# Performance work log

Hardware: AMD Instinct MI355X
Metric: run time of the kernel (lower is better)

The kernel has to match this reference:

```python
import jax, jax.numpy as jnp
import numpy as np

B, CIN, H, W = 16, 15, 256, 256
C, L, M = 64, 4, 16
ENV, D1D = 40, 4
HEAD_IN = C + ENV + D1D
BN_EPS = 1e-5


def setup_inputs() -> dict:
    key = jax.random.key(0)
    ks = iter(jax.random.split(key, 40))
    nrm = lambda shape: jax.random.normal(next(ks), shape, dtype=jnp.float32)
    scale = (2.0 / (C + C)) ** 0.5
    uni = lambda shape: scale * (jax.random.uniform(next(ks), shape, dtype=jnp.float32) - 0.5)
    d = {
        'grid': nrm((B, CIN, H, W)),
        'env': nrm((B, ENV)),
        'd1d': nrm((B, D1D)),
        'lift_w': nrm((C, CIN)) * 0.1, 'lift_b': nrm((C,)) * 0.01,
        'w1r': uni((L, C, C, M, M)), 'w1i': uni((L, C, C, M, M)),
        'w2r': uni((L, C, C, M, M)), 'w2i': uni((L, C, C, M, M)),
        'skip_w': nrm((L, C, C)) * 0.1, 'skip_b': nrm((L, C)) * 0.01,
        'bn_g': jnp.ones((L, C)), 'bn_b': jnp.zeros((L, C)),
        'bn_m': nrm((L, C)) * 0.01, 'bn_v': jnp.abs(nrm((L, C))) * 0.1 + 1.0,
        'proj_w': nrm((C, C)) * 0.1, 'proj_b': nrm((C,)) * 0.01,
        'dw1': nrm((128, HEAD_IN)) * 0.05, 'db1': nrm((128,)) * 0.01,
        'dw2': nrm((64, 128)) * 0.05, 'db2': nrm((64,)) * 0.01,
        'dw3': nrm((8, 64)) * 0.05, 'db3': nrm((8,)) * 0.01,
        'iw1': nrm((128, HEAD_IN)) * 0.05, 'ib1': nrm((128,)) * 0.01,
        'iw2': nrm((64, 128)) * 0.05, 'ib2': nrm((64,)) * 0.01,
        'iw3': nrm((4, 64)) * 0.05, 'ib3': nrm((4,)) * 0.01,
    }
    return d


def _spectral(x, w1, w2):
    # x: [B,C,H,W] real; w1,w2: [C,C,M,M] complex
    h, w = x.shape[-2], x.shape[-1]
    xft = jnp.fft.rfft2(x)  # [B,C,H,W//2+1] complex
    top = jnp.einsum('bixy,ioxy->boxy', xft[:, :, :M, :M], w1)
    bot = jnp.einsum('bixy,ioxy->boxy', xft[:, :, -M:, :M], w2)
    out_ft = jnp.zeros(xft.shape, dtype=xft.dtype)
    out_ft = out_ft.at[:, :, :M, :M].set(top).at[:, :, h - M:, :M].set(bot)
    return jnp.fft.irfft2(out_ft, s=(h, w))


def _conv1x1(x, w, b):
    return jnp.einsum('bchw,oc->bohw', x, w) + b[None, :, None, None]


def _gelu(x):
    return jax.nn.gelu(x, approximate=False)


def reference(grid, env, d1d, lift_w, lift_b, w1r, w1i, w2r, w2i, skip_w, skip_b,
              bn_g, bn_b, bn_m, bn_v, proj_w, proj_b,
              dw1, db1, dw2, db2, dw3, db3, iw1, ib1, iw2, ib2, iw3, ib3):
    x = _gelu(_conv1x1(grid, lift_w, lift_b))
    for l in range(L):
        residual = x
        w1 = w1r[l] + 1j * w1i[l]
        w2 = w2r[l] + 1j * w2i[l]
        y = _spectral(x, w1, w2) + _conv1x1(x, skip_w[l], skip_b[l])
        # BatchNorm2d in eval mode (running stats), dropout is identity at eval
        y = (y - bn_m[l][None, :, None, None]) * jax.lax.rsqrt(bn_v[l] + BN_EPS)[None, :, None, None]
        y = y * bn_g[l][None, :, None, None] + bn_b[l][None, :, None, None]
        x = _gelu(y) + residual
    x = _gelu(_conv1x1(x, proj_w, proj_b))
    x = x.mean(axis=(-2, -1))  # [B,C]
    x = jnp.concatenate([x, env, d1d], axis=-1)  # [B, C+44]
    h = _gelu(x @ dw1.T + db1)
    h = _gelu(h @ dw2.T + db2)
    out_dir = h @ dw3.T + db3
    g = _gelu(x @ iw1.T + ib1)
    g = _gelu(g @ iw2.T + ib2)
    out_int = g @ iw3.T + ib3
    return out_dir, out_int
```

## Files before the change

### kernel.cpp

```cpp
#include <hip/hip_runtime.h>
#include <hip/hip_bf16.h>
#include <math.h>

#define B_ 16
#define CIN_ 15
#define C_ 64
#define L_ 4

typedef __attribute__((ext_vector_type(8))) short short8;
typedef __attribute__((ext_vector_type(4))) float f32x4;

__device__ __forceinline__ float gelu_f(float x) {
    float z = fabsf(x) * 0.70710678118654752440f;
    float t = __builtin_amdgcn_rcpf(fmaf(0.3275911f, z, 1.0f));
    float p = t * fmaf(t, fmaf(t, fmaf(t, fmaf(t, 1.061405429f, -1.453152027f), 1.421413741f), -0.284496736f), 0.254829592f);
    float e = __expf(-z * z);
    float E = fmaf(-p, e, 1.0f);
    return 0.5f * fmaf(fabsf(x), E, x);
}

__device__ __forceinline__ unsigned short f2bf(float x) {
    __hip_bfloat16 h = __float2bfloat16(x);
    return *(unsigned short*)&h;
}
__device__ __forceinline__ float bf2f(unsigned short u) {
    __hip_bfloat16 h = *(__hip_bfloat16*)&u;
    return __bfloat162float(h);
}
__device__ __forceinline__ f32x4 mfma16(short8 a, short8 b, f32x4 c) {
    return __builtin_amdgcn_mfma_f32_16x16x32_bf16(a, b, c, 0, 0, 0);
}

#define TWO_PI_OVER_256 0.024543692606170259674f

__global__ __launch_bounds__(256) void k_prep(const float* __restrict__ skip_w,
                                              const float* __restrict__ bn_g, const float* __restrict__ bn_v,
                                              const float* __restrict__ proj_w,
                                              unsigned short* __restrict__ TfH, unsigned short* __restrict__ TfL,
                                              unsigned short* __restrict__ TiH, unsigned short* __restrict__ TiL,
                                              unsigned short* __restrict__ WH, unsigned short* __restrict__ WL,
                                              unsigned short* __restrict__ PH, unsigned short* __restrict__ PL) {
    int id = blockIdx.x * 256 + threadIdx.x;
    if (id < 8192) {
        int col = id >> 8, w = id & 255;
        int kk = (col < 16) ? col : (col - 16);
        float s, c;
        sincosf(TWO_PI_OVER_256 * (float)((w * kk) & 255), &s, &c);
        float v = (col < 16) ? c : -s;
        unsigned short hi = f2bf(v);
        TfH[id] = hi; TfL[id] = f2bf(v - bf2f(hi));
    } else if (id < 16384) {
        int idx = id - 8192;
        int w = idx >> 5, k = idx & 31, ky = k >> 1;
        float s, c;
        sincosf(TWO_PI_OVER_256 * (float)((w * ky) & 255), &s, &c);
        float v = (k & 1) ? -s : c;
        unsigned short hi = f2bf(v);
        TiH[idx] = hi; TiL[idx] = f2bf(v - bf2f(hi));
    } else if (id < 32768) {
        int idx = id - 16384;
        int lco = idx >> 6;
        float scl = bn_g[lco] * rsqrtf(bn_v[lco] + 1e-5f);
        float v = scl * skip_w[idx];
        unsigned short hi = f2bf(v);
        WH[idx] = hi; WL[idx] = f2bf(v - bf2f(hi));
    } else if (id < 36864) {
        int idx = id - 32768;
        float v = proj_w[idx];
        unsigned short hi = f2bf(v);
        PH[idx] = hi; PL[idx] = f2bf(v - bf2f(hi));
    }
}

__global__ __launch_bounds__(256) void k_lift(const float* __restrict__ g, const float* __restrict__ lw,
                                              const float* __restrict__ lb, unsigned short* __restrict__ X,
                                              const unsigned short* __restrict__ TfH, const unsigned short* __restrict__ TfL,
                                              float2* __restrict__ Y) {
    __shared__ float gs[CIN_][256];
    __shared__ float lws[C_ * CIN_];
    __shared__ float lbs[C_];
    __shared__ unsigned short xl[64 * 264];
    int b = blockIdx.x >> 8, h = blockIdx.x & 255;
    int t = threadIdx.x;
    for (int ci = 0; ci < CIN_; ci++)
        gs[ci][t] = g[((b * CIN_ + ci) * 256 + h) * 256 + t];
    for (int idx = t; idx < C_ * CIN_; idx += 256) lws[idx] = lw[idx];
    if (t < C_) lbs[t] = lb[t];
    __syncthreads();
    for (int co = 0; co < C_; co++) {
        float acc = lbs[co];
        #pragma unroll
        for (int ci = 0; ci < CIN_; ci++) acc += gs[ci][t] * lws[co * CIN_ + ci];
        xl[co * 264 + t] = f2bf(gelu_f(acc));
    }
    __syncthreads();
    {
        int wv = t >> 6, ln = t & 63;
        int lx = ln & 15, q = ln >> 4;
        f32x4 fa0 = {0.f, 0.f, 0.f, 0.f}, fa1 = {0.f, 0.f, 0.f, 0.f};
        for (int ks = 0; ks < 8; ks++) {
            int k0 = ks * 32;
            short8 a = *(const short8*)(&xl[(wv * 16 + lx) * 264 + k0 + q * 8]);
            short8 bh0 = *(const short8*)(TfH + lx * 256 + k0 + q * 8);
            short8 bl0 = *(const short8*)(TfL + lx * 256 + k0 + q * 8);
            short8 bh1 = *(const short8*)(TfH + (16 + lx) * 256 + k0 + q * 8);
            short8 bl1 = *(const short8*)(TfL + (16 + lx) * 256 + k0 + q * 8);
            fa0 = mfma16(a, bh0, fa0); fa0 = mfma16(a, bl0, fa0);
            fa1 = mfma16(a, bh1, fa1); fa1 = mfma16(a, bl1, fa1);
        }
        #pragma unroll
        for (int r = 0; r < 4; r++) {
            int c = wv * 16 + q * 4 + r;
            Y[(b * 64 + c) * 4096 + h * 16 + lx] = make_float2(fa0[r], fa1[r]);
        }
    }
    unsigned short* Xg = X + (size_t)(b * 64) * 65536 + h * 256;
    #pragma unroll
    for (int r = 0; r < 8; r++) {
        int idx = r * 256 + t;
        int c = idx >> 5, w8 = idx & 31;
        *(short8*)(Xg + c * 65536 + w8 * 8) = *(const short8*)(&xl[c * 264 + w8 * 8]);
    }
}

__global__ __launch_bounds__(256) void k_fwd_h(const float2* __restrict__ Y, float2* __restrict__ XF) {
    __shared__ float2 yl[4096];
    __shared__ float tc[256], ts[256];
    int bc = blockIdx.x;
    int t = threadIdx.x;
    {
        float s, c;
        sincosf((float)t * TWO_PI_OVER_256, &s, &c);
        tc[t] = c; ts[t] = s;
    }
    for (int idx = t; idx < 4096; idx += 256) yl[idx] = Y[bc * 4096 + idx];
    __syncthreads();
    int j = t & 31, kg = t >> 5;
    int kxu = j + ((j < 16) ? 0 : 224);
    int b = bc >> 6, c = bc & 63;
    for (int q = 0; q < 2; q++) {
        int ky = kg * 2 + q;
        float xre = 0.f, xim = 0.f;
        int m = 0;
        #pragma unroll 8
        for (int h = 0; h < 256; h++) {
            float2 yv = yl[h * 16 + ky];
            float cc = tc[m], ss = ts[m];
            xre += yv.x * cc + yv.y * ss;
            xim += yv.y * cc - yv.x * ss;
            m = (m + kxu) & 255;
        }
        XF[(j * 16 + ky) * 1024 + b * 64 + c] = make_float2(xre, xim);
    }
}

__global__ __launch_bounds__(256) void k_repack(const float* __restrict__ w1r, const float* __restrict__ w1i,
                                                const float* __restrict__ w2r, const float* __restrict__ w2i,
                                                float2* __restrict__ WPK, int l) {
    int id = blockIdx.x * 256 + threadIdx.x;
    int ky = id & 15;
    int o  = (id >> 4) & 63;
    int i  = (id >> 10) & 63;
    int j  = id >> 16;
    int x  = j & 15;
    const float* wr = (j < 16) ? w1r : w2r;
    const float* wi = (j < 16) ? w1i : w2i;
    int src = ((l * 64 + i) * 64 + o) * 256 + x * 16 + ky;
    int dst = ((j * 16 + ky) * 64 + i) * 64 + o;
    WPK[dst] = make_float2(wr[src], wi[src]);
}

__global__ __launch_bounds__(256) void k_mix(const float2* __restrict__ XF, const float2* __restrict__ WPK,
                                             float2* __restrict__ YF) {
    __shared__ float2 xs[1024];
    __shared__ float2 wls[4096];
    int s = blockIdx.x;
    int t = threadIdx.x;
    for (int idx = t; idx < 1024; idx += 256) xs[idx] = XF[s * 1024 + idx];
    for (int idx = t; idx < 4096; idx += 256) wls[idx] = WPK[(size_t)s * 4096 + idx];
    __syncthreads();
    int o = t & 63, bg = t >> 6;
    float2 acc[4];
    #pragma unroll
    for (int q = 0; q < 4; q++) acc[q] = make_float2(0.f, 0.f);
    for (int i = 0; i < 64; i++) {
        float2 wv = wls[i * 64 + o];
        #pragma unroll
        for (int q = 0; q < 4; q++) {
            float2 xv = xs[(bg * 4 + q) * 64 + i];
            acc[q].x += xv.x * wv.x - xv.y * wv.y;
            acc[q].y += xv.x * wv.y + xv.y * wv.x;
        }
    }
    #pragma unroll
    for (int q = 0; q < 4; q++) {
        int b = bg * 4 + q;
        YF[(b * 64 + o) * 512 + s] = acc[q];
    }
}

__global__ __launch_bounds__(256) void k_inv_h(const float2* __restrict__ YF, float2* __restrict__ Z) {
    __shared__ float2 yl[512];
    __shared__ float tc[256], ts[256];
    int bc = blockIdx.x, t = threadIdx.x;
    {
        float s, c;
        sincosf((float)t * TWO_PI_OVER_256, &s, &c);
        tc[t] = c; ts[t] = s;
    }
    for (int idx = t; idx < 512; idx += 256) yl[idx] = YF[bc * 512 + idx];
    __syncthreads();
    float zr[16], zi[16];
    #pragma unroll
    for (int ky = 0; ky < 16; ky++) { zr[ky] = 0.f; zi[ky] = 0.f; }
    for (int j = 0; j < 32; j++) {
        int kxu = j + ((j < 16) ? 0 : 224);
        int m = (t * kxu) & 255;
        float cc = tc[m], ss = ts[m];
        #pragma unroll
        for (int ky = 0; ky < 16; ky++) {
            float2 yv = yl[j * 16 + ky];
            zr[ky] += yv.x * cc - yv.y * ss;
            zi[ky] += yv.x * ss + yv.y * cc;
        }
    }
    int base = bc * 4096 + t * 16;
    #pragma unroll
    for (int ky = 0; ky < 16; ky++) Z[base + ky] = make_float2(zr[ky], zi[ky]);
}

__global__ __launch_bounds__(256) void k_tail(unsigned short* __restrict__ X, const float2* __restrict__ Z,
                                              const unsigned short* __restrict__ WH, const unsigned short* __restrict__ WL,
                                              const float* __restrict__ sbl, const float* __restrict__ bng,
                                              const float* __restrict__ bnb, const float* __restrict__ bnm,
                                              const float* __restrict__ bnv,
                                              const unsigned short* __restrict__ TiH, const unsigned short* __restrict__ TiL,
                                              const unsigned short* __restrict__ TfH, const unsigned short* __restrict__ TfL,
                                              float2* __restrict__ Y, int mode,
                                              const unsigned short* __restrict__ PH, const unsigned short* __restrict__ PL,
                                              const float* __restrict__ pb, float* __restrict__ ACC) {
    __shared__ unsigned short xl[64 * 264];
    __shared__ float cbs[64];
    __shared__ float pacc[64];
    __shared__ float pbs[64];
    int b = blockIdx.x >> 8, h = blockIdx.x & 255;
    int t = threadIdx.x;
    unsigned short* Xg = X + (size_t)(b * 64) * 65536 + h * 256;
    #pragma unroll
    for (int r = 0; r < 8; r++) {
        int idx = r * 256 + t;
        int c = idx >> 5, w8 = idx & 31;
        *(short8*)(&xl[c * 264 + w8 * 8]) = *(const short8*)(Xg + c * 65536 + w8 * 8);
    }
    if (t < 64) {
        float scl = bng[t] * rsqrtf(bnv[t] + 1e-5f);
        cbs[t] = scl * (sbl[t] - bnm[t]) + bnb[t];
        pacc[t] = 0.f;
        pbs[t] = pb[t];
    }
    __syncthreads();

    int wv = t >> 6, ln = t & 63;
    int lx = ln & 15, q = ln >> 4;

    short8 azh[4], azl[4];
    {
        const float2* Zg = Z + (size_t)(b * 64) * 4096 + h * 16;
        #pragma unroll
        for (int mt = 0; mt < 4; mt++) {
            int co = mt * 16 + lx;
            float scl = bng[co] * rsqrtf(bnv[co] + 1e-5f);
            float f2v = scl * (2.0f / 65536.0f);
            float f0 = (q == 0) ? (scl * (1.0f / 65536.0f)) : f2v;
            const float4* zp = (const float4*)(Zg + (size_t)co * 4096 + q * 4);
            float4 z0 = zp[0], z1 = zp[1];
            float v[8];
            v[0] = z0.x * f0;  v[1] = z0.y * f0;
            v[2] = z0.z * f2v; v[3] = z0.w * f2v;
            v[4] = z1.x * f2v; v[5] = z1.y * f2v;
            v[6] = z1.z * f2v; v[7] = z1.w * f2v;
            #pragma unroll
            for (int j = 0; j < 8; j++) {
                unsigned short hv = f2bf(v[j]);
                azh[mt][j] = (short)hv;
                azl[mt][j] = (short)f2bf(v[j] - bf2f(hv));
            }
        }
    }

    #pragma unroll 1
    for (int nt = 0; nt < 4; nt++) {
        int w = wv * 64 + nt * 16 + lx;
        f32x4 acc[4];
        #pragma unroll
        for (int mt = 0; mt < 4; mt++) acc[mt] = (f32x4){0.f, 0.f, 0.f, 0.f};
        {
            short8 tbh = *(const short8*)(TiH + w * 32 + q * 8);
            short8 tbl = *(const short8*)(TiL + w * 32 + q * 8);
            #pragma unroll
            for (int mt = 0; mt < 4; mt++) {
                acc[mt] = mfma16(azh[mt], tbh, acc[mt]);
                acc[mt] = mfma16(azh[mt], tbl, acc[mt]);
                acc[mt] = mfma16(azl[mt], tbh, acc[mt]);
            }
        }
        #pragma unroll
        for (int ks = 0; ks < 2; ks++) {
            int k0 = ks * 32;
            short8 bfr;
            #pragma unroll
            for (int j = 0; j < 8; j++)
                bfr[j] = (short)xl[(k0 + q * 8 + j) * 264 + w];
            #pragma unroll
            for (int mt = 0; mt < 4; mt++) {
                short8 ah = *(const short8*)(WH + (mt * 16 + lx) * 64 + k0 + q * 8);
                short8 al = *(const short8*)(WL + (mt * 16 + lx) * 64 + k0 + q * 8);
                acc[mt] = mfma16(ah, bfr, acc[mt]);
                acc[mt] = mfma16(al, bfr, acc[mt]);
            }
        }
        #pragma unroll
        for (int mt = 0; mt < 4; mt++) {
            #pragma unroll
            for (int r = 0; r < 4; r++) {
                int co = mt * 16 + q * 4 + r;
                float y = acc[mt][r] + cbs[co];
                float v = gelu_f(y) + bf2f(xl[co * 264 + w]);
                xl[co * 264 + w] = f2bf(v);
            }
        }
    }
    __syncthreads();

    if (mode == 1) {
        f32x4 fa0 = {0.f, 0.f, 0.f, 0.f}, fa1 = {0.f, 0.f, 0.f, 0.f};
        for (int ks = 0; ks < 8; ks++) {
            int k0 = ks * 32;
            short8 a = *(const short8*)(&xl[(wv * 16 + lx) * 264 + k0 + q * 8]);
            short8 bh0 = *(const short8*)(TfH + lx * 256 + k0 + q * 8);
            short8 bl0 = *(const short8*)(TfL + lx * 256 + k0 + q * 8);
            short8 bh1 = *(const short8*)(TfH + (16 + lx) * 256 + k0 + q * 8);
            short8 bl1 = *(const short8*)(TfL + (16 + lx) * 256 + k0 + q * 8);
            fa0 = mfma16(a, bh0, fa0); fa0 = mfma16(a, bl0, fa0);
            fa1 = mfma16(a, bh1, fa1); fa1 = mfma16(a, bl1, fa1);
        }
        #pragma unroll
        for (int r = 0; r < 4; r++) {
            int c = wv * 16 + q * 4 + r;
            Y[(b * 64 + c) * 4096 + h * 16 + lx] = make_float2(fa0[r], fa1[r]);
        }
        #pragma unroll
        for (int r = 0; r < 8; r++) {
            int idx = r * 256 + t;
            int c = idx >> 5, w8 = idx & 31;
            *(short8*)(Xg + c * 65536 + w8 * 8) = *(const short8*)(&xl[c * 264 + w8 * 8]);
        }
    } else {
        float psum[4][4];
        #pragma unroll
        for (int mt = 0; mt < 4; mt++)
            #pragma unroll
            for (int r = 0; r < 4; r++) psum[mt][r] = 0.f;
        #pragma unroll 1
        for (int nt = 0; nt < 4; nt++) {
            int w = wv * 64 + nt * 16 + lx;
            f32x4 acc[4];
            #pragma unroll
            for (int mt = 0; mt < 4; mt++) acc[mt] = (f32x4){0.f, 0.f, 0.f, 0.f};
            #pragma unroll
            for (int ks = 0; ks < 2; ks++) {
                int k0 = ks * 32;
                short8 bfr;
                #pragma unroll
                for (int j = 0; j < 8; j++)
                    bfr[j] = (short)xl[(k0 + q * 8 + j) * 264 + w];
                #pragma unroll
                for (int mt = 0; mt < 4; mt++) {
                    short8 ah = *(const short8*)(PH + (mt * 16 + lx) * 64 + k0 + q * 8);
                    short8 al = *(const short8*)(PL + (mt * 16 + lx) * 64 + k0 + q * 8);
                    acc[mt] = mfma16(ah, bfr, acc[mt]);
                    acc[mt] = mfma16(al, bfr, acc[mt]);
                }
            }
            #pragma unroll
            for (int mt = 0; mt < 4; mt++)
                #pragma unroll
                for (int r = 0; r < 4; r++) {
                    int co = mt * 16 + q * 4 + r;
                    psum[mt][r] += gelu_f(acc[mt][r] + pbs[co]);
                }
        }
        #pragma unroll
        for (int mt = 0; mt < 4; mt++) {
            #pragma unroll
            for (int r = 0; r < 4; r++) {
                int co = mt * 16 + q * 4 + r;
                float s = psum[mt][r];
                s += __shfl_xor(s, 1, 64);
                s += __shfl_xor(s, 2, 64);
                s += __shfl_xor(s, 4, 64);
                s += __shfl_xor(s, 8, 64);
                if (lx == 0) atomicAdd(&pacc[co], s);
            }
        }
        __syncthreads();
        if (t < 64) atomicAdd(&ACC[b * 64 + t], pacc[t]);
    }
}

__global__ __launch_bounds__(128) void k_head(const float* __restrict__ ACC, const float* __restrict__ env,
                                              const float* __restrict__ d1d,
                                              const float* __restrict__ dw1, const float* __restrict__ db1,
                                              const float* __restrict__ dw2, const float* __restrict__ db2,
                                              const float* __restrict__ dw3, const float* __restrict__ db3,
                                              const float* __restrict__ iw1, const float* __restrict__ ib1,
                                              const float* __restrict__ iw2, const float* __restrict__ ib2,
                                              const float* __restrict__ iw3, const float* __restrict__ ib3,
                                              float* __restrict__ out) {
    __shared__ float xc[108];
    __shared__ float h1[128];
    __shared__ float h2[64];
    int b = blockIdx.x, t = threadIdx.x;
    if (t < 64) xc[t] = ACC[b * 64 + t] * (1.0f / 65536.0f);
    else if (t < 104) xc[t] = env[b * 40 + (t - 64)];
    else if (t < 108) xc[t] = d1d[b * 4 + (t - 104)];
    __syncthreads();
    {
        float a = db1[t];
        for (int k = 0; k < 108; k++) a += xc[k] * dw1[t * 108 + k];
        h1[t] = gelu_f(a);
    }
    __syncthreads();
    if (t < 64) {
        float a = db2[t];
        for (int k = 0; k < 128; k++) a += h1[k] * dw2[t * 128 + k];
        h2[t] = gelu_f(a);
    }
    __syncthreads();
    if (t < 8) {
        float a = db3[t];
        for (int k = 0; k < 64; k++) a += h2[k] * dw3[t * 64 + k];
        out[b * 8 + t] = a;
    }
    __syncthreads();
    {
        float a = ib1[t];
        for (int k = 0; k < 108; k++) a += xc[k] * iw1[t * 108 + k];
        h1[t] = gelu_f(a);
    }
    __syncthreads();
    if (t < 64) {
        float a = ib2[t];
        for (int k = 0; k < 128; k++) a += h1[k] * iw2[t * 128 + k];
        h2[t] = gelu_f(a);
    }
    __syncthreads();
    if (t < 4) {
        float a = ib3[t];
        for (int k = 0; k < 64; k++) a += h2[k] * iw3[t * 64 + k];
        out[128 + b * 4 + t] = a;
    }
}

extern "C" void kernel_launch(void* const* d_in, const int* in_sizes, int n_in,
                              void* d_out, int out_size, void* d_ws, size_t ws_size,
                              hipStream_t stream) {
    const float* grid_  = (const float*)d_in[0];
    const float* env    = (const float*)d_in[1];
    const float* d1d    = (const float*)d_in[2];
    const float* lift_w = (const float*)d_in[3];
    const float* lift_b = (const float*)d_in[4];
    const float* w1r    = (const float*)d_in[5];
    const float* w1i    = (const float*)d_in[6];
    const float* w2r    = (const float*)d_in[7];
    const float* w2i    = (const float*)d_in[8];
    const float* skip_w = (const float*)d_in[9];
    const float* skip_b = (const float*)d_in[10];
    const float* bn_g   = (const float*)d_in[11];
    const float* bn_b   = (const float*)d_in[12];
    const float* bn_m   = (const float*)d_in[13];
    const float* bn_v   = (const float*)d_in[14];
    const float* proj_w = (const float*)d_in[15];
    const float* proj_b = (const float*)d_in[16];
    const float* dw1 = (const float*)d_in[17];
    const float* db1 = (const float*)d_in[18];
    const float* dw2 = (const float*)d_in[19];
    const float* db2 = (const float*)d_in[20];
    const float* dw3 = (const float*)d_in[21];
    const float* db3 = (const float*)d_in[22];
    const float* iw1 = (const float*)d_in[23];
    const float* ib1 = (const float*)d_in[24];
    const float* iw2 = (const float*)d_in[25];
    const float* ib2 = (const float*)d_in[26];
    const float* iw3 = (const float*)d_in[27];
    const float* ib3 = (const float*)d_in[28];

    char* ws = (char*)d_ws;
    unsigned short* X   = (unsigned short*)(ws);
    float2* S   = (float2*)(ws + 134217728);
    float2* XF  = (float2*)(ws + 167772160);
    float2* YF  = (float2*)(ws + 171966464);
    float2* WPK = (float2*)(ws + 176160768);
    float*  ACC = (float*)(ws + 192937984);
    unsigned short* TfH = (unsigned short*)(ws + 192942080);
    unsigned short* TfL = (unsigned short*)(ws + 192958464);
    unsigned short* TiH = (unsigned short*)(ws + 192974848);
    unsigned short* TiL = (unsigned short*)(ws + 192991232);
    unsigned short* WH  = (unsigned short*)(ws + 193007616);
    unsigned short* WL  = (unsigned short*)(ws + 193040384);
    unsigned short* PH  = (unsigned short*)(ws + 193073152);
    unsigned short* PL  = (unsigned short*)(ws + 193081344);

    hipMemsetAsync(ACC, 0, 1024 * sizeof(float), stream);
    k_prep<<<144, 256, 0, stream>>>(skip_w, bn_g, bn_v, proj_w, TfH, TfL, TiH, TiL, WH, WL, PH, PL);
    k_lift<<<4096, 256, 0, stream>>>(grid_, lift_w, lift_b, X, TfH, TfL, S);
    for (int l = 0; l < L_; l++) {
        k_repack<<<8192, 256, 0, stream>>>(w1r, w1i, w2r, w2i, WPK, l);
        k_fwd_h<<<1024, 256, 0, stream>>>(S, XF);
        k_mix<<<512, 256, 0, stream>>>(XF, WPK, YF);
        k_inv_h<<<1024, 256, 0, stream>>>(YF, S);
        k_tail<<<4096, 256, 0, stream>>>(X, S, WH + l * 4096, WL + l * 4096,
                                         skip_b + l * 64, bn_g + l * 64, bn_b + l * 64,
                                         bn_m + l * 64, bn_v + l * 64,
                                         TiH, TiL, TfH, TfL, S, (l < 3) ? 1 : 2,
                                         PH, PL, proj_b, ACC);
    }
    k_head<<<16, 128, 0, stream>>>(ACC, env, d1d, dw1, db1, dw2, db2, dw3, db3,
                                   iw1, ib1, iw2, ib2, iw3, ib3, (float*)d_out);
}
```

Baseline: 1.380 ms.

## Move H-axis partial DFTs onto bf16 MFMA with split-precision twiddle tables

The forward and inverse H-direction DFT kernels are rewritten from scalar FMA loops over LDS twiddles to bf16x3 split-precision MFMA matrix products. The cos, sin and negated-sin twiddle matrices are precomputed in hi/lo bf16 form by the prep kernel. The forward kernel splits the 256-long H reduction across four waves and sums their partials in shared memory. The weight repack kernel is also changed to process four outputs per thread with vectorized float4 stores. The goal is to cut FP32 ALU time in the DFT stages, at the cost of extra precomputed tables and bf16 split rounding error.

```diff
diff --git a/kernel.cpp b/kernel.cpp
--- a/kernel.cpp
+++ b/kernel.cpp
@@ -39,7 +39,13 @@
                                               unsigned short* __restrict__ TfH, unsigned short* __restrict__ TfL,
                                               unsigned short* __restrict__ TiH, unsigned short* __restrict__ TiL,
                                               unsigned short* __restrict__ WH, unsigned short* __restrict__ WL,
-                                              unsigned short* __restrict__ PH, unsigned short* __restrict__ PL) {
+                                              unsigned short* __restrict__ PH, unsigned short* __restrict__ PL,
+                                              unsigned short* __restrict__ FcH, unsigned short* __restrict__ FcL,
+                                              unsigned short* __restrict__ FsH, unsigned short* __restrict__ FsL,
+                                              unsigned short* __restrict__ FnH, unsigned short* __restrict__ FnL,
+                                              unsigned short* __restrict__ IcH, unsigned short* __restrict__ IcL,
+                                              unsigned short* __restrict__ IsH, unsigned short* __restrict__ IsL,
+                                              unsigned short* __restrict__ InH, unsigned short* __restrict__ InL) {
     int id = blockIdx.x * 256 + threadIdx.x;
     if (id < 8192) {
         int col = id >> 8, w = id & 255;
@@ -69,6 +75,30 @@
         float v = proj_w[idx];
         unsigned short hi = f2bf(v);
         PH[idx] = hi; PL[idx] = f2bf(v - bf2f(hi));
+    } else if (id < 45056) {
+        int idx = id - 36864;
+        int j = idx >> 8, h = idx & 255;
+        int kxu = j + ((j < 16) ? 0 : 224);
+        float s, c;
+        sincosf(TWO_PI_OVER_256 * (float)((h * kxu) & 255), &s, &c);
+        unsigned short ch = f2bf(c);
+        FcH[idx] = ch; FcL[idx] = f2bf(c - bf2f(ch));
+        unsigned short sh = f2bf(s);
+        unsigned short sl = f2bf(s - bf2f(sh));
+        FsH[idx] = sh; FsL[idx] = sl;
+        FnH[idx] = sh ^ 0x8000; FnL[idx] = sl ^ 0x8000;
+    } else if (id < 53248) {
+        int idx = id - 45056;
+        int h = idx >> 5, j = idx & 31;
+        int kxu = j + ((j < 16) ? 0 : 224);
+        float s, c;
+        sincosf(TWO_PI_OVER_256 * (float)((h * kxu) & 255), &s, &c);
+        unsigned short ch = f2bf(c);
+        IcH[idx] = ch; IcL[idx] = f2bf(c - bf2f(ch));
+        unsigned short sh = f2bf(s);
+        unsigned short sl = f2bf(s - bf2f(sh));
+        IsH[idx] = sh; IsL[idx] = sl;
+        InH[idx] = sh ^ 0x8000; InL[idx] = sl ^ 0x8000;
     }
 }
 
@@ -123,51 +153,93 @@
     }
 }
 
-__global__ __launch_bounds__(256) void k_fwd_h(const float2* __restrict__ Y, float2* __restrict__ XF) {
-    __shared__ float2 yl[4096];
-    __shared__ float tc[256], ts[256];
+__global__ __launch_bounds__(256) void k_fwd_h(const float2* __restrict__ Y, float2* __restrict__ XF,
+                                               const unsigned short* __restrict__ FcH, const unsigned short* __restrict__ FcL,
+                                               const unsigned short* __restrict__ FsH, const unsigned short* __restrict__ FsL,
+                                               const unsigned short* __restrict__ FnH, const unsigned short* __restrict__ FnL) {
+    __shared__ float red[4][2][2][64][4];
     int bc = blockIdx.x;
     int t = threadIdx.x;
-    {
-        float s, c;
-        sincosf((float)t * TWO_PI_OVER_256, &s, &c);
-        tc[t] = c; ts[t] = s;
-    }
-    for (int idx = t; idx < 4096; idx += 256) yl[idx] = Y[bc * 4096 + idx];
-    __syncthreads();
-    int j = t & 31, kg = t >> 5;
-    int kxu = j + ((j < 16) ? 0 : 224);
-    int b = bc >> 6, c = bc & 63;
-    for (int q = 0; q < 2; q++) {
-        int ky = kg * 2 + q;
-        float xre = 0.f, xim = 0.f;
-        int m = 0;
-        #pragma unroll 8
-        for (int h = 0; h < 256; h++) {
-            float2 yv = yl[h * 16 + ky];
-            float cc = tc[m], ss = ts[m];
-            xre += yv.x * cc + yv.y * ss;
-            xim += yv.y * cc - yv.x * ss;
-            m = (m + kxu) & 255;
-        }
-        XF[(j * 16 + ky) * 1024 + b * 64 + c] = make_float2(xre, xim);
+    int wv = t >> 6, l = t & 63, lx = l & 15, g = l >> 4;
+    const float2* Yb = Y + (size_t)bc * 4096;
+    f32x4 aR[2], aI[2];
+    aR[0] = (f32x4){0.f,0.f,0.f,0.f}; aR[1] = aR[0]; aI[0] = aR[0]; aI[1] = aR[0];
+    #pragma unroll
+    for (int kk = 0; kk < 2; kk++) {
+        int ks = wv * 2 + kk;
+        short8 yrh, yrl, yih, yil;
+        #pragma unroll
+        for (int j = 0; j < 8; j++) {
+            float2 v = Yb[(ks * 32 + g * 8 + j) * 16 + lx];
+            unsigned short h1 = f2bf(v.x);
+            yrh[j] = (short)h1; yrl[j] = (short)f2bf(v.x - bf2f(h1));
+            unsigned short h2 = f2bf(v.y);
+            yih[j] = (short)h2; yil[j] = (short)f2bf(v.y - bf2f(h2));
+        }
+        #pragma unroll
+        for (int rt = 0; rt < 2; rt++) {
+            int base = (rt * 16 + lx) * 256 + ks * 32 + g * 8;
+            short8 ch = *(const short8*)(FcH + base);
+            short8 cl = *(const short8*)(FcL + base);
+            short8 sh = *(const short8*)(FsH + base);
+            short8 sl = *(const short8*)(FsL + base);
+            short8 nh = *(const short8*)(FnH + base);
+            short8 nl = *(const short8*)(FnL + base);
+            aR[rt] = mfma16(ch, yrh, aR[rt]);
+            aR[rt] = mfma16(ch, yrl, aR[rt]);
+            aR[rt] = mfma16(cl, yrh, aR[rt]);
+            aR[rt] = mfma16(sh, yih, aR[rt]);
+            aR[rt] = mfma16(sh, yil, aR[rt]);
+            aR[rt] = mfma16(sl, yih, aR[rt]);
+            aI[rt] = mfma16(ch, yih, aI[rt]);
+            aI[rt] = mfma16(ch, yil, aI[rt]);
+            aI[rt] = mfma16(cl, yih, aI[rt]);
+            aI[rt] = mfma16(nh, yrh, aI[rt]);
+            aI[rt] = mfma16(nh, yrl, aI[rt]);
+            aI[rt] = mfma16(nl, yrh, aI[rt]);
+        }
+    }
+    #pragma unroll
+    for (int rt = 0; rt < 2; rt++) {
+        *(f32x4*)&red[wv][rt][0][l][0] = aR[rt];
+        *(f32x4*)&red[wv][rt][1][l][0] = aI[rt];
+    }
+    __syncthreads();
+    if (t < 128) {
+        int rt = t >> 6, ll = t & 63;
+        int llx = ll & 15, gg = ll >> 4;
+        f32x4 R = *(const f32x4*)&red[0][rt][0][ll][0];
+        f32x4 I = *(const f32x4*)&red[0][rt][1][ll][0];
+        #pragma unroll
+        for (int w = 1; w < 4; w++) {
+            R += *(const f32x4*)&red[w][rt][0][ll][0];
+            I += *(const f32x4*)&red[w][rt][1][ll][0];
+        }
+        #pragma unroll
+        for (int r = 0; r < 4; r++) {
+            int j = rt * 16 + gg * 4 + r;
+            XF[(j * 16 + llx) * 1024 + bc] = make_float2(R[r], I[r]);
+        }
     }
 }
 
 __global__ __launch_bounds__(256) void k_repack(const float* __restrict__ w1r, const float* __restrict__ w1i,
                                                 const float* __restrict__ w2r, const float* __restrict__ w2i,
                                                 float2* __restrict__ WPK, int l) {
-    int id = blockIdx.x * 256 + threadIdx.x;
-    int ky = id & 15;
-    int o  = (id >> 4) & 63;
-    int i  = (id >> 10) & 63;
-    int j  = id >> 16;
-    int x  = j & 15;
+    int j = blockIdx.x >> 6, i = blockIdx.x & 63;
+    int t = threadIdx.x;
+    int ky = t & 15, o0 = (t >> 4) * 4;
+    int x = j & 15;
     const float* wr = (j < 16) ? w1r : w2r;
     const float* wi = (j < 16) ? w1i : w2i;
-    int src = ((l * 64 + i) * 64 + o) * 256 + x * 16 + ky;
-    int dst = ((j * 16 + ky) * 64 + i) * 64 + o;
-    WPK[dst] = make_float2(wr[src], wi[src]);
+    size_t sb = ((size_t)(l * 64 + i) * 64 + o0) * 256 + x * 16 + ky;
+    float r0 = wr[sb];       float v0 = wi[sb];
+    float r1 = wr[sb + 256]; float v1 = wi[sb + 256];
+    float r2 = wr[sb + 512]; float v2 = wi[sb + 512];
+    float r3 = wr[sb + 768]; float v3 = wi[sb + 768];
+    float4* dst = (float4*)(WPK + ((size_t)(j * 16 + ky) * 64 + i) * 64 + o0);
+    dst[0] = make_float4(r0, v0, r1, v1);
+    dst[1] = make_float4(r2, v2, r3, v3);
 }
 
 __global__ __launch_bounds__(256) void k_mix(const float2* __restrict__ XF, const float2* __restrict__ WPK,
@@ -199,34 +271,45 @@
     }
 }
 
-__global__ __launch_bounds__(256) void k_inv_h(const float2* __restrict__ YF, float2* __restrict__ Z) {
-    __shared__ float2 yl[512];
-    __shared__ float tc[256], ts[256];
-    int bc = blockIdx.x, t = threadIdx.x;
-    {
-        float s, c;
-        sincosf((float)t * TWO_PI_OVER_256, &s, &c);
-        tc[t] = c; ts[t] = s;
-    }
-    for (int idx = t; idx < 512; idx += 256) yl[idx] = YF[bc * 512 + idx];
-    __syncthreads();
-    float zr[16], zi[16];
-    #pragma unroll
-    for (int ky = 0; ky < 16; ky++) { zr[ky] = 0.f; zi[ky] = 0.f; }
-    for (int j = 0; j < 32; j++) {
-        int kxu = j + ((j < 16) ? 0 : 224);
-        int m = (t * kxu) & 255;
-        float cc = tc[m], ss = ts[m];
-        #pragma unroll
-        for (int ky = 0; ky < 16; ky++) {
-            float2 yv = yl[j * 16 + ky];
-            zr[ky] += yv.x * cc - yv.y * ss;
-            zi[ky] += yv.x * ss + yv.y * cc;
-        }
-    }
-    int base = bc * 4096 + t * 16;
-    #pragma unroll
-    for (int ky = 0; ky < 16; ky++) Z[base + ky] = make_float2(zr[ky], zi[ky]);
+__global__ __launch_bounds__(256) void k_inv_h(const float2* __restrict__ YF, float2* __restrict__ Z,
+                                               const unsigned short* __restrict__ IcH, const unsigned short* __restrict__ IcL,
+                                               const unsigned short* __restrict__ IsH, const unsigned short* __restrict__ IsL,
+                                               const unsigned short* __restrict__ InH, const unsigned short* __restrict__ InL) {
+    int bc = blockIdx.x;
+    int t = threadIdx.x;
+    int wv = t >> 6, l = t & 63, lx = l & 15, g = l >> 4;
+    const float2* Yb = YF + (size_t)bc * 512;
+    short8 xrh, xrl, xih, xil;
+    #pragma unroll
+    for (int jj = 0; jj < 8; jj++) {
+        float2 v = Yb[(g * 8 + jj) * 16 + lx];
+        unsigned short h1 = f2bf(v.x);
+        xrh[jj] = (short)h1; xrl[jj] = (short)f2bf(v.x - bf2f(h1));
+        unsigned short h2 = f2bf(v.y);
+        xih[jj] = (short)h2; xil[jj] = (short)f2bf(v.y - bf2f(h2));
+    }
+    float2* Zb = Z + (size_t)bc * 4096;
+    #pragma unroll
+    for (int hh = 0; hh < 4; hh++) {
+        int ht = wv * 4 + hh;
+        int base = (ht * 16 + lx) * 32 + g * 8;
+        short8 ch = *(const short8*)(IcH + base);
+        short8 cl = *(const short8*)(IcL + base);
+        short8 sh = *(const short8*)(IsH + base);
+        short8 sl = *(const short8*)(IsL + base);
+        short8 nh = *(const short8*)(InH + base);
+        short8 nl = *(const short8*)(InL + base);
+        f32x4 aR = {0.f,0.f,0.f,0.f}, aI = {0.f,0.f,0.f,0.f};
+        aR = mfma16(ch, xrh, aR); aR = mfma16(ch, xrl, aR); aR = mfma16(cl, xrh, aR);
+        aR = mfma16(nh, xih, aR); aR = mfma16(nh, xil, aR); aR = mfma16(nl, xih, aR);
+        aI = mfma16(sh, xrh, aI); aI = mfma16(sh, xrl, aI); aI = mfma16(sl, xrh, aI);
+        aI = mfma16(ch, xih, aI); aI = mfma16(ch, xil, aI); aI = mfma16(cl, xih, aI);
+        #pragma unroll
+        for (int r = 0; r < 4; r++) {
+            int h = ht * 16 + g * 4 + r;
+            Zb[h * 16 + lx] = make_float2(aR[r], aI[r]);
+        }
+    }
 }
 
 __global__ __launch_bounds__(256) void k_tail(unsigned short* __restrict__ X, const float2* __restrict__ Z,
@@ -510,15 +593,28 @@
     unsigned short* WL  = (unsigned short*)(ws + 193040384);
     unsigned short* PH  = (unsigned short*)(ws + 193073152);
     unsigned short* PL  = (unsigned short*)(ws + 193081344);
+    unsigned short* FcH = (unsigned short*)(ws + 193089536);
+    unsigned short* FcL = (unsigned short*)(ws + 193105920);
+    unsigned short* FsH = (unsigned short*)(ws + 193122304);
+    unsigned short* FsL = (unsigned short*)(ws + 193138688);
+    unsigned short* FnH = (unsigned short*)(ws + 193155072);
+    unsigned short* FnL = (unsigned short*)(ws + 193171456);
+    unsigned short* IcH = (unsigned short*)(ws + 193187840);
+    unsigned short* IcL = (unsigned short*)(ws + 193204224);
+    unsigned short* IsH = (unsigned short*)(ws + 193220608);
+    unsigned short* IsL = (unsigned short*)(ws + 193236992);
+    unsigned short* InH = (unsigned short*)(ws + 193253376);
+    unsigned short* InL = (unsigned short*)(ws + 193269760);
 
     hipMemsetAsync(ACC, 0, 1024 * sizeof(float), stream);
-    k_prep<<<144, 256, 0, stream>>>(skip_w, bn_g, bn_v, proj_w, TfH, TfL, TiH, TiL, WH, WL, PH, PL);
+    k_prep<<<208, 256, 0, stream>>>(skip_w, bn_g, bn_v, proj_w, TfH, TfL, TiH, TiL, WH, WL, PH, PL,
+                                    FcH, FcL, FsH, FsL, FnH, FnL, IcH, IcL, IsH, IsL, InH, InL);
     k_lift<<<4096, 256, 0, stream>>>(grid_, lift_w, lift_b, X, TfH, TfL, S);
     for (int l = 0; l < L_; l++) {
-        k_repack<<<8192, 256, 0, stream>>>(w1r, w1i, w2r, w2i, WPK, l);
-        k_fwd_h<<<1024, 256, 0, stream>>>(S, XF);
+        k_repack<<<2048, 256, 0, stream>>>(w1r, w1i, w2r, w2i, WPK, l);
+        k_fwd_h<<<1024, 256, 0, stream>>>(S, XF, FcH, FcL, FsH, FsL, FnH, FnL);
         k_mix<<<512, 256, 0, stream>>>(XF, WPK, YF);
-        k_inv_h<<<1024, 256, 0, stream>>>(YF, S);
+        k_inv_h<<<1024, 256, 0, stream>>>(YF, S, IcH, IcL, IsH, IsL, InH, InL);
         k_tail<<<4096, 256, 0, stream>>>(X, S, WH + l * 4096, WL + l * 4096,
                                          skip_b + l * 64, bn_g + l * 64, bn_b + l * 64,
                                          bn_m + l * 64, bn_v + l * 64,
```

Measured after the change: 1.161 ms. -15.9%, faster.
